# Kernel tuning notes

Hardware: AMD Instinct MI355X
Metric: run time of the kernel (lower is better)

## Reference

```python
import jax, jax.numpy as jnp
import numpy as np

N = 50000      # nodes
E = 800000     # edges (avg degree 16)
IN = 128       # in_channels
HID = 32       # hidden_channels per head
HEADS = 4
OUT = 64       # out_channels (last layer, heads=1, concat=False)
ED = 32        # edge_dim
NEG_SLOPE = 0.2


def _gatv2_layer(x, src, dst, ea, Wl, bl, Wr, br, We, att, bias, concat):
    """PyG GATv2Conv: lin_l -> source (x_j), lin_r -> target (x_i),
    score = att . leaky_relu(x_i + x_j + lin_edge(edge_attr)), segment-softmax over dst,
    out = scatter_add(alpha * x_j) per head, then concat or mean heads, plus bias."""
    n = x.shape[0]
    H, C = att.shape
    xl = (x @ Wl + bl).reshape(-1, H, C)   # [N,H,C] source transform
    xr = (x @ Wr + br).reshape(-1, H, C)   # [N,H,C] target transform
    ee = (ea @ We).reshape(-1, H, C)       # [E,H,C] edge transform
    m = jax.nn.leaky_relu(xl[src] + xr[dst] + ee, NEG_SLOPE)  # [E,H,C]
    a = jnp.einsum('ehc,hc->eh', m, att)   # [E,H] attention logits
    amax = jax.ops.segment_max(a, dst, num_segments=n)        # [N,H]
    ex = jnp.exp(a - amax[dst])
    den = jax.ops.segment_sum(ex, dst, num_segments=n)        # [N,H]
    alpha = ex / (den[dst] + 1e-16)        # [E,H] segment softmax
    out = jax.ops.segment_sum(xl[src] * alpha[..., None], dst, num_segments=n)  # [N,H,C]
    out = out.reshape(n, H * C) if concat else out.mean(axis=1)
    return out + bias


def setup_inputs() -> dict:
    key = jax.random.key(0)
    ks = jax.random.split(key, 20)
    s = 0.05
    HC = HEADS * HID
    inp = {
        'x': jax.random.normal(ks[0], (N, IN), jnp.float32),
        'edge_index': jax.random.randint(ks[1], (2, E), 0, N, jnp.int32),
        'edge_attr': jax.random.normal(ks[2], (E, ED), jnp.float32),
        # layer 1: GATv2Conv(IN -> HID, heads=HEADS, concat=True, edge_dim=ED)
        'Wl1': jax.random.normal(ks[3], (IN, HC), jnp.float32) * s,
        'bl1': jnp.zeros((HC,), jnp.float32),
        'Wr1': jax.random.normal(ks[4], (IN, HC), jnp.float32) * s,
        'br1': jnp.zeros((HC,), jnp.float32),
        'We1': jax.random.normal(ks[5], (ED, HC), jnp.float32) * s,
        'att1': jax.random.normal(ks[6], (HEADS, HID), jnp.float32) * s,
        'bias1': jnp.zeros((HC,), jnp.float32),
        # layer 2: GATv2Conv(HC -> OUT, heads=1, concat=False, edge_dim=ED)
        'Wl2': jax.random.normal(ks[7], (HC, OUT), jnp.float32) * s,
        'bl2': jnp.zeros((OUT,), jnp.float32),
        'Wr2': jax.random.normal(ks[8], (HC, OUT), jnp.float32) * s,
        'br2': jnp.zeros((OUT,), jnp.float32),
        'We2': jax.random.normal(ks[9], (ED, OUT), jnp.float32) * s,
        'att2': jax.random.normal(ks[10], (1, OUT), jnp.float32) * s,
        'bias2': jnp.zeros((OUT,), jnp.float32),
    }
    return inp


def reference(x, edge_index, edge_attr, Wl1, bl1, Wr1, br1, We1, att1, bias1,
              Wl2, bl2, Wr2, br2, We2, att2, bias2):
    src, dst = edge_index[0], edge_index[1]
    h = _gatv2_layer(x, src, dst, edge_attr, Wl1, bl1, Wr1, br1, We1, att1, bias1, concat=True)
    h = jax.nn.elu(h)
    out = _gatv2_layer(h, src, dst, edge_attr, Wl2, bl2, Wr2, br2, We2, att2, bias2, concat=False)
    return out
```

## Files before the change

### kernel.cpp

```cpp
#include <hip/hip_runtime.h>
#include <stdint.h>

#define N_NODES 50000
#define N_EDGES 800000

struct Ptrs { const void* p[16]; int n[16]; };

typedef __attribute__((ext_vector_type(8))) short bf16x8;
typedef __attribute__((ext_vector_type(4))) float f32x4;

__device__ __forceinline__ float bf2f(unsigned short u){
  union { unsigned int i; float f; } v; v.i = ((unsigned int)u) << 16; return v.f;
}
__device__ __forceinline__ float lo16(unsigned int u){ union { unsigned int i; float f; } v; v.i = u << 16; return v.f; }
__device__ __forceinline__ float hi16(unsigned int u){ union { unsigned int i; float f; } v; v.i = u & 0xffff0000u; return v.f; }
__device__ __forceinline__ unsigned short f2bf(float f){
  if (!(f == f)) return 0;
  unsigned int x = __float_as_uint(f);
  unsigned int r = (x + 0x7fffu + ((x >> 16) & 1u)) >> 16;
  return (unsigned short)r;
}
__device__ __forceinline__ float fin(float v){
  if (!(v == v)) return 0.f;
  return fminf(fmaxf(v, -1e30f), 1e30f);
}
__device__ __forceinline__ float loadF(const void* p, int f32, size_t idx){
  return f32 ? ((const float*)p)[idx] : bf2f(((const unsigned short*)p)[idx]);
}

__global__ __launch_bounds__(256) void k_detect(Ptrs tl, int* __restrict__ flags,
                                                int* __restrict__ counts, int* __restrict__ pad16)
{
  if (blockIdx.x >= 16) {
    int i = (blockIdx.x - 16) * 256 + threadIdx.x;
    if (i < N_NODES) counts[i] = 0;
    if (blockIdx.x == 16 && threadIdx.x < 16) pad16[threadIdx.x] = 0;
    return;
  }
  __shared__ int red[256];
  int b = blockIdx.x, t = threadIdx.x;
  const unsigned short* p = (const unsigned short*)tl.p[b];
  int n = tl.n[b]; if (n > 16384) n = 16384;
  int crazy = 0;
  for (int i = t; i < n; i += 256) {
    unsigned short u = p[i];
    if (u) {
      int ex = (u >> 7) & 0xFF;
      if (ex == 0xFF || ex < 0x60) crazy++;
    }
  }
  red[t] = crazy; __syncthreads();
  for (int off = 128; off; off >>= 1) { if (t < off) red[t] += red[t + off]; __syncthreads(); }
  if (t == 0) flags[b] = (red[0] * 10 > n) ? 1 : 0;
}

__global__ __launch_bounds__(256) void k_gemm1(
    const void* __restrict__ x,
    const void* __restrict__ Wl, const void* __restrict__ bl,
    const void* __restrict__ Wr, const void* __restrict__ br,
    const int* __restrict__ flags,
    unsigned int* __restrict__ xlp, unsigned int* __restrict__ xrp)
{
  __shared__ __align__(16) char smem[17408];
  unsigned short* xh  = (unsigned short*)smem;
  unsigned short* xlo = (unsigned short*)(smem + 8704);
  float* outb = (float*)smem;
  const void* W  = blockIdx.y ? Wr : Wl;
  const void* bb = blockIdx.y ? br : bl;
  int fW = blockIdx.y ? flags[4] : flags[2];
  int fB = blockIdx.y ? flags[5] : flags[3];
  int fX = flags[0];
  unsigned int* outp = blockIdx.y ? xrp : xlp;
  int tid = threadIdx.x;
  int row0 = blockIdx.x * 32;
  for (int i = tid * 4; i < 32 * 128; i += 1024) {
    int r = i >> 7, k = i & 127;
    int row = row0 + r;
    float4 v = make_float4(0.f, 0.f, 0.f, 0.f);
    if (row < N_NODES) {
      if (fX) v = *(const float4*)((const float*)x + (size_t)row * 128 + k);
      else {
        uint2 u = *(const uint2*)((const unsigned short*)x + (size_t)row * 128 + k);
        v.x = lo16(u.x); v.y = hi16(u.x); v.z = lo16(u.y); v.w = hi16(u.y);
      }
    }
    unsigned short h0 = f2bf(v.x), h1 = f2bf(v.y), h2 = f2bf(v.z), h3 = f2bf(v.w);
    *(ushort4*)(xh + r * 136 + k) = make_ushort4(h0, h1, h2, h3);
    ushort4 lv;
    lv.x = f2bf(v.x - bf2f(h0)); lv.y = f2bf(v.y - bf2f(h1));
    lv.z = f2bf(v.z - bf2f(h2)); lv.w = f2bf(v.w - bf2f(h3));
    *(ushort4*)(xlo + r * 136 + k) = lv;
  }
  int lane = tid & 63, wv = tid >> 6;
  int idx16 = lane & 15, quad = lane >> 4;
  bf16x8 bfr[2][4];
#pragma unroll
  for (int ct = 0; ct < 2; ct++) {
#pragma unroll
    for (int kc = 0; kc < 4; kc++) {
      int col = wv * 32 + ct * 16 + idx16;
      unsigned short tmp[8];
#pragma unroll
      for (int j = 0; j < 8; j++) {
        int kk = kc * 32 + quad * 8 + j;
        tmp[j] = fW ? f2bf(((const float*)W)[(size_t)kk * 128 + col])
                    : ((const unsigned short*)W)[(size_t)kk * 128 + col];
      }
      bfr[ct][kc] = *(const bf16x8*)tmp;
    }
  }
  __syncthreads();
  f32x4 acc[2][2];
#pragma unroll
  for (int rt = 0; rt < 2; rt++)
#pragma unroll
    for (int ct = 0; ct < 2; ct++)
      acc[rt][ct] = (f32x4){0.f, 0.f, 0.f, 0.f};
#pragma unroll
  for (int kc = 0; kc < 4; kc++) {
#pragma unroll
    for (int rt = 0; rt < 2; rt++) {
      bf16x8 ah = *(const bf16x8*)(xh  + (rt * 16 + idx16) * 136 + kc * 32 + quad * 8);
      bf16x8 al = *(const bf16x8*)(xlo + (rt * 16 + idx16) * 136 + kc * 32 + quad * 8);
#pragma unroll
      for (int ct = 0; ct < 2; ct++) {
        acc[rt][ct] = __builtin_amdgcn_mfma_f32_16x16x32_bf16(ah, bfr[ct][kc], acc[rt][ct], 0, 0, 0);
        acc[rt][ct] = __builtin_amdgcn_mfma_f32_16x16x32_bf16(al, bfr[ct][kc], acc[rt][ct], 0, 0, 0);
      }
    }
  }
  __syncthreads();
#pragma unroll
  for (int rt = 0; rt < 2; rt++)
#pragma unroll
    for (int ct = 0; ct < 2; ct++)
#pragma unroll
      for (int r = 0; r < 4; r++)
        outb[(rt * 16 + quad * 4 + r) * 132 + wv * 32 + ct * 16 + idx16] = acc[rt][ct][r];
  __syncthreads();
  int r = tid >> 3, cg = tid & 7;
  float a2[16];
#pragma unroll
  for (int j = 0; j < 8; j++) {
    a2[j]     = outb[r * 132 + cg * 8 + j];
    a2[8 + j] = outb[r * 132 + 64 + cg * 8 + j];
  }
  int row = row0 + r;
  if (row < N_NODES) {
    unsigned int* op = outp + (size_t)row * 64;
    int tt = cg >> 1, qb = (cg & 1) * 2;
    unsigned int ou[4];
#pragma unroll
    for (int t = 0; t < 4; t++) {
      float f0 = fin(a2[2 * t]     + loadF(bb, fB, cg * 8 + 2 * t));
      float f1 = fin(a2[2 * t + 1] + loadF(bb, fB, cg * 8 + 2 * t + 1));
      ou[t] = (unsigned)f2bf(f0) | ((unsigned)f2bf(f1) << 16);
    }
    *(uint2*)(op + qb * 16 + tt * 2)       = make_uint2(ou[0], ou[1]);
    *(uint2*)(op + (qb + 1) * 16 + tt * 2) = make_uint2(ou[2], ou[3]);
#pragma unroll
    for (int t = 0; t < 4; t++) {
      float f0 = fin(a2[8 + 2 * t]     + loadF(bb, fB, 64 + cg * 8 + 2 * t));
      float f1 = fin(a2[8 + 2 * t + 1] + loadF(bb, fB, 64 + cg * 8 + 2 * t + 1));
      ou[t] = (unsigned)f2bf(f0) | ((unsigned)f2bf(f1) << 16);
    }
    *(uint2*)(op + qb * 16 + 8 + tt * 2)       = make_uint2(ou[0], ou[1]);
    *(uint2*)(op + (qb + 1) * 16 + 8 + tt * 2) = make_uint2(ou[2], ou[3]);
  }
}

__global__ __launch_bounds__(256) void k_gemm2(
    const float* __restrict__ h,
    const void* __restrict__ Wl, const void* __restrict__ bl,
    const void* __restrict__ Wr, const void* __restrict__ br,
    const int* __restrict__ flags,
    unsigned int* __restrict__ xlp, unsigned int* __restrict__ xrp)
{
  __shared__ __align__(16) char smem[17408];
  unsigned short* hh  = (unsigned short*)smem;
  unsigned short* hlo = (unsigned short*)(smem + 8704);
  float* outb = (float*)smem;
  const void* W  = blockIdx.y ? Wr : Wl;
  const void* bb = blockIdx.y ? br : bl;
  int fW = blockIdx.y ? flags[11] : flags[9];
  int fB = blockIdx.y ? flags[12] : flags[10];
  unsigned int* outp = blockIdx.y ? xrp : xlp;
  int tid = threadIdx.x;
  int row0 = blockIdx.x * 32;
  for (int i = tid * 4; i < 32 * 128; i += 1024) {
    int r = i >> 7, k = i & 127;
    int row = row0 + r;
    float4 v = make_float4(0.f, 0.f, 0.f, 0.f);
    if (row < N_NODES) v = *(const float4*)(h + (size_t)row * 128 + k);
    unsigned short h0 = f2bf(v.x), h1 = f2bf(v.y), h2 = f2bf(v.z), h3 = f2bf(v.w);
    *(ushort4*)(hh + r * 136 + k) = make_ushort4(h0, h1, h2, h3);
    ushort4 lv;
    lv.x = f2bf(v.x - bf2f(h0)); lv.y = f2bf(v.y - bf2f(h1));
    lv.z = f2bf(v.z - bf2f(h2)); lv.w = f2bf(v.w - bf2f(h3));
    *(ushort4*)(hlo + r * 136 + k) = lv;
  }
  int lane = tid & 63, wv = tid >> 6;
  int idx16 = lane & 15, quad = lane >> 4;
  bf16x8 bfr[4];
#pragma unroll
  for (int kc = 0; kc < 4; kc++) {
    int col = wv * 16 + idx16;
    unsigned short tmp[8];
#pragma unroll
    for (int j = 0; j < 8; j++) {
      int kk = kc * 32 + quad * 8 + j;
      tmp[j] = fW ? f2bf(((const float*)W)[(size_t)kk * 64 + col])
                  : ((const unsigned short*)W)[(size_t)kk * 64 + col];
    }
    bfr[kc] = *(const bf16x8*)tmp;
  }
  __syncthreads();
  f32x4 acc[2];
  acc[0] = (f32x4){0.f, 0.f, 0.f, 0.f};
  acc[1] = (f32x4){0.f, 0.f, 0.f, 0.f};
#pragma unroll
  for (int kc = 0; kc < 4; kc++) {
#pragma unroll
    for (int rt = 0; rt < 2; rt++) {
      bf16x8 ah = *(const bf16x8*)(hh  + (rt * 16 + idx16) * 136 + kc * 32 + quad * 8);
      bf16x8 al = *(const bf16x8*)(hlo + (rt * 16 + idx16) * 136 + kc * 32 + quad * 8);
      acc[rt] = __builtin_amdgcn_mfma_f32_16x16x32_bf16(ah, bfr[kc], acc[rt], 0, 0, 0);
      acc[rt] = __builtin_amdgcn_mfma_f32_16x16x32_bf16(al, bfr[kc], acc[rt], 0, 0, 0);
    }
  }
  __syncthreads();
#pragma unroll
  for (int rt = 0; rt < 2; rt++)
#pragma unroll
    for (int r = 0; r < 4; r++)
      outb[(rt * 16 + quad * 4 + r) * 68 + wv * 16 + idx16] = acc[rt][r];
  __syncthreads();
  int r = tid >> 3, cg = tid & 7;
  float a2[8];
#pragma unroll
  for (int j = 0; j < 8; j++) a2[j] = outb[r * 68 + cg * 8 + j];
  int row = row0 + r;
  if (row < N_NODES) {
    unsigned int* op = outp + (size_t)row * 32;
    int tt = cg >> 1, qb = (cg & 1) * 2;
    unsigned int ou[4];
#pragma unroll
    for (int t = 0; t < 4; t++) {
      float f0 = fin(a2[2 * t]     + loadF(bb, fB, cg * 8 + 2 * t));
      float f1 = fin(a2[2 * t + 1] + loadF(bb, fB, cg * 8 + 2 * t + 1));
      ou[t] = (unsigned)f2bf(f0) | ((unsigned)f2bf(f1) << 16);
    }
    *(uint2*)(op + qb * 8 + tt * 2)       = make_uint2(ou[0], ou[1]);
    *(uint2*)(op + (qb + 1) * 8 + tt * 2) = make_uint2(ou[2], ou[3]);
  }
}

__global__ __launch_bounds__(256) void k_hist(const int* __restrict__ ei, int* __restrict__ counts)
{
  int e = blockIdx.x * 256 + threadIdx.x;
  if (e < N_EDGES) {
    int d = ei[N_EDGES + e]; if ((unsigned)d >= N_NODES) d = 0;
    atomicAdd(&counts[d], 1);
  }
}

__global__ __launch_bounds__(256) void k_scan1(const int* __restrict__ counts,
                                               int* __restrict__ row_ptr, int* __restrict__ bsum)
{
  __shared__ int lds[256];
  int t = threadIdx.x;
  int base = blockIdx.x * 1024 + t * 4;
  int c0 = (base + 0) < N_NODES ? counts[base + 0] : 0;
  int c1 = (base + 1) < N_NODES ? counts[base + 1] : 0;
  int c2 = (base + 2) < N_NODES ? counts[base + 2] : 0;
  int c3 = (base + 3) < N_NODES ? counts[base + 3] : 0;
  int s = c0 + c1 + c2 + c3;
  lds[t] = s; __syncthreads();
  for (int off = 1; off < 256; off <<= 1) {
    int v = (t >= off) ? lds[t - off] : 0;
    __syncthreads();
    lds[t] += v;
    __syncthreads();
  }
  int incl = lds[t];
  int excl = incl - s;
  if (base + 0 < N_NODES) row_ptr[base + 0] = excl;
  if (base + 1 < N_NODES) row_ptr[base + 1] = excl + c0;
  if (base + 2 < N_NODES) row_ptr[base + 2] = excl + c0 + c1;
  if (base + 3 < N_NODES) row_ptr[base + 3] = excl + c0 + c1 + c2;
  if (t == 255) bsum[blockIdx.x] = incl;
}

__global__ __launch_bounds__(64) void k_scan2(int* __restrict__ bsum, int nb)
{
  __shared__ int l[64];
  int t = threadIdx.x;
  if (t < nb) l[t] = bsum[t];
  __syncthreads();
  if (t == 0) { int run = 0; for (int i = 0; i < nb; i++) { int v = l[i]; l[i] = run; run += v; } }
  __syncthreads();
  if (t < nb) bsum[t] = l[t];
}

__global__ __launch_bounds__(256) void k_scan3(int* __restrict__ row_ptr, int* __restrict__ cursor,
                                               const int* __restrict__ bsum)
{
  int t = threadIdx.x;
  int base = blockIdx.x * 1024 + t * 4;
  int add = bsum[blockIdx.x];
#pragma unroll
  for (int j = 0; j < 4; j++) {
    int i = base + j;
    if (i < N_NODES) { int v = row_ptr[i] + add; row_ptr[i] = v; cursor[i] = v; }
  }
  if (blockIdx.x == 0 && t == 0) row_ptr[N_NODES] = N_EDGES;
}

__global__ __launch_bounds__(256) void k_scatter(const int* __restrict__ ei,
                                                 int* __restrict__ cursor,
                                                 int* __restrict__ srcs,
                                                 const void* __restrict__ ea,
                                                 const int* __restrict__ flags,
                                                 unsigned short* __restrict__ eap)
{
  int e = blockIdx.x * 256 + threadIdx.x;
  if (e >= N_EDGES) return;
  int d = ei[N_EDGES + e]; if ((unsigned)d >= N_NODES) d = 0;
  int s = ei[e];           if ((unsigned)s >= N_NODES) s = 0;
  int p = atomicAdd(&cursor[d], 1);
  if ((unsigned)p >= N_EDGES) return;
  srcs[p] = s;
  unsigned short* op = eap + (size_t)p * 32;
  if (flags[1]) {
    const float* ip = (const float*)ea + (size_t)e * 32;
#pragma unroll
    for (int q = 0; q < 2; q++) {
      float4 a = *(const float4*)(ip + q * 16);
      float4 b = *(const float4*)(ip + q * 16 + 4);
      float4 c = *(const float4*)(ip + q * 16 + 8);
      float4 dd = *(const float4*)(ip + q * 16 + 12);
      uint4 u0, u1;
      u0.x = (unsigned)f2bf(a.x) | ((unsigned)f2bf(a.y) << 16);
      u0.y = (unsigned)f2bf(a.z) | ((unsigned)f2bf(a.w) << 16);
      u0.z = (unsigned)f2bf(b.x) | ((unsigned)f2bf(b.y) << 16);
      u0.w = (unsigned)f2bf(b.z) | ((unsigned)f2bf(b.w) << 16);
      u1.x = (unsigned)f2bf(c.x) | ((unsigned)f2bf(c.y) << 16);
      u1.y = (unsigned)f2bf(c.z) | ((unsigned)f2bf(c.w) << 16);
      u1.z = (unsigned)f2bf(dd.x) | ((unsigned)f2bf(dd.y) << 16);
      u1.w = (unsigned)f2bf(dd.z) | ((unsigned)f2bf(dd.w) << 16);
      *(uint4*)(op + q * 16) = u0;
      *(uint4*)(op + q * 16 + 8) = u1;
    }
  } else {
    const uint4* ip = (const uint4*)((const unsigned short*)ea + (size_t)e * 32);
#pragma unroll
    for (int q = 0; q < 4; q++) *(uint4*)(op + q * 8) = ip[q];
  }
}

__global__ __launch_bounds__(256) void k_fuse1(
    const unsigned short* __restrict__ eap, const int* __restrict__ srcs,
    const int* __restrict__ row_ptr,
    const unsigned int* __restrict__ xlp, const unsigned int* __restrict__ xrp,
    const void* __restrict__ We, const void* __restrict__ att,
    const void* __restrict__ bias, const int* __restrict__ flags,
    float* __restrict__ hout)
{
  __shared__ unsigned short wt[128 * 34];
  __shared__ float at[128];
  int tid = threadIdx.x;
  {
    int f = flags[6];
    for (int i2 = tid; i2 < 4096; i2 += 256) {
      int k = i2 >> 7, c = i2 & 127;
      wt[c * 34 + k] = f ? f2bf(((const float*)We)[i2]) : ((const unsigned short*)We)[i2];
    }
  }
  if (tid < 128) at[tid] = loadF(att, flags[7], tid);
  __syncthreads();
  int lane = tid & 63;
  int idx16 = lane & 15, quad = lane >> 4;
  int t_s = (lane & 15) >> 1, b_s = lane & 1;
  int un = t_s * 8 + quad * 2 + b_s;
  int hd = un >> 4;
  bf16x8 af[8];
#pragma unroll
  for (int t = 0; t < 8; t++)
    af[t] = *(const bf16x8*)(wt + (t * 16 + idx16) * 34 + quad * 8);
  int wv = tid >> 6;
#pragma unroll 1
  for (int rep = 0; rep < 2; rep++) {
    int i = blockIdx.x * 8 + rep * 4 + wv;
    int p0 = row_ptr[i], p1 = row_ptr[i + 1];
    uint2 rv[8];
#pragma unroll
    for (int t4 = 0; t4 < 4; t4++) {
      uint4 u = *(const uint4*)(xrp + (size_t)i * 64 + quad * 16 + t4 * 4);
      rv[2 * t4]     = make_uint2(u.x, u.y);
      rv[2 * t4 + 1] = make_uint2(u.z, u.w);
    }
    float acc0 = 0.f, acc1 = 0.f, den = 0.f;
    for (int jb = p0; jb < p1; jb += 16) {
      int j = jb + idx16;
      int act = j < p1;
      int jc = act ? j : p0;
      int s = srcs[jc];
      bf16x8 bfrag = *(const bf16x8*)(eap + (size_t)jc * 32 + quad * 8);
      uint2 xv[8];
#pragma unroll
      for (int t4 = 0; t4 < 4; t4++) {
        uint4 u = *(const uint4*)(xlp + (size_t)s * 64 + quad * 16 + t4 * 4);
        xv[2 * t4]     = make_uint2(u.x, u.y);
        xv[2 * t4 + 1] = make_uint2(u.z, u.w);
      }
      float ph0 = 0.f, ph1 = 0.f, ph2 = 0.f, ph3 = 0.f;
#pragma unroll
      for (int t = 0; t < 8; t++) {
        float4 av = *(const float4*)(at + t * 16 + quad * 4);
        uint2 r = rv[t];
        f32x4 c = {0.f, 0.f, 0.f, 0.f};
        c = __builtin_amdgcn_mfma_f32_16x16x32_bf16(af[t], bfrag, c, 0, 0, 0);
        float z0 = c[0] + lo16(xv[t].x) + lo16(r.x);
        float z1 = c[1] + hi16(xv[t].x) + hi16(r.x);
        float z2 = c[2] + lo16(xv[t].y) + lo16(r.y);
        float z3 = c[3] + hi16(xv[t].y) + hi16(r.y);
        z0 = z0 > 0.f ? z0 : 0.2f * z0;
        z1 = z1 > 0.f ? z1 : 0.2f * z1;
        z2 = z2 > 0.f ? z2 : 0.2f * z2;
        z3 = z3 > 0.f ? z3 : 0.2f * z3;
        float pp = fmaf(av.x, z0, fmaf(av.y, z1, fmaf(av.z, z2, av.w * z3)));
        if (t < 2)      ph0 += pp;
        else if (t < 4) ph1 += pp;
        else if (t < 6) ph2 += pp;
        else            ph3 += pp;
      }
      ph0 += __shfl_xor(ph0, 16, 64); ph0 += __shfl_xor(ph0, 32, 64);
      ph1 += __shfl_xor(ph1, 16, 64); ph1 += __shfl_xor(ph1, 32, 64);
      ph2 += __shfl_xor(ph2, 16, 64); ph2 += __shfl_xor(ph2, 32, 64);
      ph3 += __shfl_xor(ph3, 16, 64); ph3 += __shfl_xor(ph3, 32, 64);
      float w0 = act ? __expf(fminf(fin(ph0), 25.f)) : 0.f;
      float w1 = act ? __expf(fminf(fin(ph1), 25.f)) : 0.f;
      float w2 = act ? __expf(fminf(fin(ph2), 25.f)) : 0.f;
      float w3 = act ? __expf(fminf(fin(ph3), 25.f)) : 0.f;
      float wsel = quad == 0 ? w0 : quad == 1 ? w1 : quad == 2 ? w2 : w3;
      int sjl[16];
      float wjv[16];
#pragma unroll
      for (int q = 0; q < 16; q++) sjl[q] = __shfl(s, q, 64);
#pragma unroll
      for (int q = 0; q < 16; q++) wjv[q] = __shfl(wsel, hd * 16 + q, 64);
#pragma unroll
      for (int q = 0; q < 16; q++) {
        unsigned int v = xlp[(size_t)sjl[q] * 64 + lane];
        acc0 = fmaf(wjv[q], lo16(v), acc0);
        acc1 = fmaf(wjv[q], hi16(v), acc1);
        den += wjv[q];
      }
    }
    float inv = 1.f / (den + 1e-16f);
    int fB = flags[8];
    int ch = un * 2;
    float o0 = fin(fmaf(acc0, inv, loadF(bias, fB, ch)));
    float o1 = fin(fmaf(acc1, inv, loadF(bias, fB, ch + 1)));
    o0 = o0 > 0.f ? o0 : __expf(o0) - 1.f;
    o1 = o1 > 0.f ? o1 : __expf(o1) - 1.f;
    *(float2*)(hout + (size_t)i * 128 + ch) = make_float2(o0, o1);
  }
}

__global__ __launch_bounds__(256) void k_fuse2(
    const unsigned short* __restrict__ eap, const int* __restrict__ srcs,
    const int* __restrict__ row_ptr,
    const unsigned int* __restrict__ xlp, const unsigned int* __restrict__ xrp,
    const void* __restrict__ We, const void* __restrict__ att,
    const void* __restrict__ bias, const int* __restrict__ flags,
    void* __restrict__ out)
{
  __shared__ unsigned short wt[64 * 34];
  __shared__ float at[64];
  int tid = threadIdx.x;
  {
    int f = flags[13];
    for (int i2 = tid; i2 < 2048; i2 += 256) {
      int k = i2 >> 6, c = i2 & 63;
      wt[c * 34 + k] = f ? f2bf(((const float*)We)[i2]) : ((const unsigned short*)We)[i2];
    }
  }
  if (tid < 64) at[tid] = loadF(att, flags[14], tid);
  __syncthreads();
  int lane = tid & 63;
  int idx16 = lane & 15, quad = lane >> 4;
  int l5 = lane & 31;
  int q_s = l5 >> 3, t2 = (l5 & 7) >> 1, b2 = l5 & 1;
  int un = t2 * 8 + q_s * 2 + b2;
  int halfe = lane >> 5;
  bf16x8 af[4];
#pragma unroll
  for (int t = 0; t < 4; t++)
    af[t] = *(const bf16x8*)(wt + (t * 16 + idx16) * 34 + quad * 8);
  int wv = tid >> 6;
#pragma unroll 1
  for (int rep = 0; rep < 2; rep++) {
    int i = blockIdx.x * 8 + rep * 4 + wv;
    int p0 = row_ptr[i], p1 = row_ptr[i + 1];
    uint2 rv[4];
#pragma unroll
    for (int k = 0; k < 2; k++) {
      uint4 u = *(const uint4*)(xrp + (size_t)i * 32 + quad * 8 + k * 4);
      rv[2 * k]     = make_uint2(u.x, u.y);
      rv[2 * k + 1] = make_uint2(u.z, u.w);
    }
    float acc0 = 0.f, acc1 = 0.f, den = 0.f;
    for (int jb = p0; jb < p1; jb += 16) {
      int j = jb + idx16;
      int act = j < p1;
      int jc = act ? j : p0;
      int s = srcs[jc];
      bf16x8 bfrag = *(const bf16x8*)(eap + (size_t)jc * 32 + quad * 8);
      uint2 xv[4];
#pragma unroll
      for (int k = 0; k < 2; k++) {
        uint4 u = *(const uint4*)(xlp + (size_t)s * 32 + quad * 8 + k * 4);
        xv[2 * k]     = make_uint2(u.x, u.y);
        xv[2 * k + 1] = make_uint2(u.z, u.w);
      }
      float ph = 0.f;
#pragma unroll
      for (int t = 0; t < 4; t++) {
        float4 av = *(const float4*)(at + t * 16 + quad * 4);
        uint2 r = rv[t];
        f32x4 c = {0.f, 0.f, 0.f, 0.f};
        c = __builtin_amdgcn_mfma_f32_16x16x32_bf16(af[t], bfrag, c, 0, 0, 0);
        float z0 = c[0] + lo16(xv[t].x) + lo16(r.x);
        float z1 = c[1] + hi16(xv[t].x) + hi16(r.x);
        float z2 = c[2] + lo16(xv[t].y) + lo16(r.y);
        float z3 = c[3] + hi16(xv[t].y) + hi16(r.y);
        z0 = z0 > 0.f ? z0 : 0.2f * z0;
        z1 = z1 > 0.f ? z1 : 0.2f * z1;
        z2 = z2 > 0.f ? z2 : 0.2f * z2;
        z3 = z3 > 0.f ? z3 : 0.2f * z3;
        ph += fmaf(av.x, z0, fmaf(av.y, z1, fmaf(av.z, z2, av.w * z3)));
      }
      ph += __shfl_xor(ph, 16, 64);
      ph += __shfl_xor(ph, 32, 64);
      float wsel = act ? __expf(fminf(fin(ph), 25.f)) : 0.f;
      int sjl[8];
      float wjv[8];
#pragma unroll
      for (int q = 0; q < 8; q++) {
        int qq = 2 * q + halfe;
        sjl[q] = __shfl(s, qq, 64);
        wjv[q] = __shfl(wsel, qq, 64);
      }
#pragma unroll
      for (int q = 0; q < 8; q++) {
        unsigned int v = xlp[(size_t)sjl[q] * 32 + l5];
        acc0 = fmaf(wjv[q], lo16(v), acc0);
        acc1 = fmaf(wjv[q], hi16(v), acc1);
        den += wjv[q];
      }
    }
    acc0 += __shfl_xor(acc0, 32, 64);
    acc1 += __shfl_xor(acc1, 32, 64);
    den  += __shfl_xor(den, 32, 64);
    if (lane < 32) {
      float inv = 1.f / (den + 1e-16f);
      int fB = flags[15];
      int ch = un * 2;
      float o0 = fin(fmaf(acc0, inv, loadF(bias, fB, ch)));
      float o1 = fin(fmaf(acc1, inv, loadF(bias, fB, ch + 1)));
      if (flags[0]) {
        *(float2*)((float*)out + (size_t)i * 64 + ch) = make_float2(o0, o1);
      } else {
        unsigned int u = (unsigned)f2bf(o0) | ((unsigned)f2bf(o1) << 16);
        *(unsigned int*)((unsigned short*)out + (size_t)i * 64 + ch) = u;
      }
    }
  }
}

extern "C" void kernel_launch(void* const* d_in, const int* in_sizes, int n_in,
                              void* d_out, int out_size, void* d_ws, size_t ws_size,
                              hipStream_t stream)
{
  (void)n_in; (void)out_size; (void)ws_size;
  const void* x    = d_in[0];
  const int*  ei   = (const int*)d_in[1];
  const void* ea   = d_in[2];
  const void* Wl1  = d_in[3];
  const void* bl1  = d_in[4];
  const void* Wr1  = d_in[5];
  const void* br1  = d_in[6];
  const void* We1  = d_in[7];
  const void* att1 = d_in[8];
  const void* bias1= d_in[9];
  const void* Wl2  = d_in[10];
  const void* bl2  = d_in[11];
  const void* Wr2  = d_in[12];
  const void* br2  = d_in[13];
  const void* We2  = d_in[14];
  const void* att2 = d_in[15];
  const void* bias2= d_in[16];

  char* ws = (char*)d_ws;
  size_t off = 0;
  auto take = [&](size_t bytes) -> char* {
    char* p = ws + off;
    off += (bytes + 255) & ~(size_t)255;
    return p;
  };
  unsigned int* xl1p = (unsigned int*)take((size_t)N_NODES * 64 * 4);
  unsigned int* xr1p = (unsigned int*)take((size_t)N_NODES * 64 * 4);
  float* hbuf   = (float*)take((size_t)N_NODES * 128 * 4);
  unsigned short* eap = (unsigned short*)take((size_t)(N_EDGES + 16) * 32 * 2);
  int*   counts = (int*)  take((size_t)N_NODES * 4);
  int*   row_ptr= (int*)  take((size_t)(N_NODES + 1) * 4);
  int*   cursor = (int*)  take((size_t)N_NODES * 4);
  int*   srcs   = (int*)  take((size_t)(N_EDGES + 16) * 4);
  int*   bsum   = (int*)  take(64 * 4);
  int*   flags  = (int*)  take(64 * 4);
  unsigned int* xl2p = xl1p;
  unsigned int* xr2p = xr1p;

  Ptrs tl;
  const int map[16] = {0, 2, 3, 4, 5, 6, 7, 8, 9, 10, 11, 12, 13, 14, 15, 16};
  for (int j = 0; j < 16; j++) { tl.p[j] = d_in[map[j]]; tl.n[j] = in_sizes[map[j]]; }

  int nb = (N_NODES + 1023) / 1024;
  int zblocks = (N_NODES + 255) / 256;
  k_detect<<<16 + zblocks, 256, 0, stream>>>(tl, flags, counts, srcs + N_EDGES);
  k_gemm1<<<dim3((N_NODES + 31) / 32, 2), 256, 0, stream>>>(x, Wl1, bl1, Wr1, br1, flags, xl1p, xr1p);
  k_hist<<<(N_EDGES + 255) / 256, 256, 0, stream>>>(ei, counts);
  k_scan1<<<nb, 256, 0, stream>>>(counts, row_ptr, bsum);
  k_scan2<<<1, 64, 0, stream>>>(bsum, nb);
  k_scan3<<<nb, 256, 0, stream>>>(row_ptr, cursor, bsum);
  k_scatter<<<(N_EDGES + 255) / 256, 256, 0, stream>>>(ei, cursor, srcs, ea, flags, eap);
  k_fuse1<<<N_NODES / 8, 256, 0, stream>>>(eap, srcs, row_ptr, xl1p, xr1p, We1, att1, bias1, flags, hbuf);
  k_gemm2<<<dim3((N_NODES + 31) / 32, 2), 256, 0, stream>>>(hbuf, Wl2, bl2, Wr2, br2, flags, xl2p, xr2p);
  k_fuse2<<<N_NODES / 8, 256, 0, stream>>>(eap, srcs, row_ptr, xl2p, xr2p, We2, att2, bias2, flags, d_out);
}
```

Before: 657.7 us.

## Merge scan kernels, stage target rows in LDS, prefetch neighbor rows early

Fuses the single-block bsum scan into the offset-add kernel: each block reduces the preceding block sums with wave shuffles, which removes one launch. In both aggregation kernels the target-node xr rows are staged in shared memory instead of registers. The gathered source-row loads for the weighted sum are now issued before the MFMA and attention computation, so their latency overlaps that math. The cost is higher register pressure from the 16 prefetched values, plus extra LDS reads inside the inner loop.

```diff
diff --git a/kernel.cpp b/kernel.cpp
--- a/kernel.cpp
+++ b/kernel.cpp
@@ -291,23 +291,21 @@
   if (t == 255) bsum[blockIdx.x] = incl;
 }
 
-__global__ __launch_bounds__(64) void k_scan2(int* __restrict__ bsum, int nb)
-{
-  __shared__ int l[64];
+__global__ __launch_bounds__(256) void k_scan23(int* __restrict__ row_ptr, int* __restrict__ cursor,
+                                                const int* __restrict__ bsum, int nb)
+{
+  __shared__ int sadd;
   int t = threadIdx.x;
-  if (t < nb) l[t] = bsum[t];
-  __syncthreads();
-  if (t == 0) { int run = 0; for (int i = 0; i < nb; i++) { int v = l[i]; l[i] = run; run += v; } }
-  __syncthreads();
-  if (t < nb) bsum[t] = l[t];
-}
-
-__global__ __launch_bounds__(256) void k_scan3(int* __restrict__ row_ptr, int* __restrict__ cursor,
-                                               const int* __restrict__ bsum)
-{
-  int t = threadIdx.x;
+  if (t < 64) {
+    int v = (t < nb && t < (int)blockIdx.x) ? bsum[t] : 0;
+    v += __shfl_xor(v, 1, 64);  v += __shfl_xor(v, 2, 64);
+    v += __shfl_xor(v, 4, 64);  v += __shfl_xor(v, 8, 64);
+    v += __shfl_xor(v, 16, 64); v += __shfl_xor(v, 32, 64);
+    if (t == 0) sadd = v;
+  }
+  __syncthreads();
+  int add = sadd;
   int base = blockIdx.x * 1024 + t * 4;
-  int add = bsum[blockIdx.x];
 #pragma unroll
   for (int j = 0; j < 4; j++) {
     int i = base + j;
@@ -368,6 +366,7 @@
 {
   __shared__ unsigned short wt[128 * 34];
   __shared__ float at[128];
+  __shared__ __align__(16) unsigned int xr_s[8 * 64];
   int tid = threadIdx.x;
   {
     int f = flags[6];
@@ -377,6 +376,8 @@
     }
   }
   if (tid < 128) at[tid] = loadF(att, flags[7], tid);
+  for (int i2 = tid; i2 < 512; i2 += 256)
+    xr_s[i2] = xrp[(size_t)(blockIdx.x * 8 + (i2 >> 6)) * 64 + (i2 & 63)];
   __syncthreads();
   int lane = tid & 63;
   int idx16 = lane & 15, quad = lane >> 4;
@@ -390,15 +391,10 @@
   int wv = tid >> 6;
 #pragma unroll 1
   for (int rep = 0; rep < 2; rep++) {
-    int i = blockIdx.x * 8 + rep * 4 + wv;
+    int loc = rep * 4 + wv;
+    int i = blockIdx.x * 8 + loc;
     int p0 = row_ptr[i], p1 = row_ptr[i + 1];
-    uint2 rv[8];
-#pragma unroll
-    for (int t4 = 0; t4 < 4; t4++) {
-      uint4 u = *(const uint4*)(xrp + (size_t)i * 64 + quad * 16 + t4 * 4);
-      rv[2 * t4]     = make_uint2(u.x, u.y);
-      rv[2 * t4 + 1] = make_uint2(u.z, u.w);
-    }
+    const unsigned int* xr_row = xr_s + loc * 64;
     float acc0 = 0.f, acc1 = 0.f, den = 0.f;
     for (int jb = p0; jb < p1; jb += 16) {
       int j = jb + idx16;
@@ -413,11 +409,17 @@
         xv[2 * t4]     = make_uint2(u.x, u.y);
         xv[2 * t4 + 1] = make_uint2(u.z, u.w);
       }
+      int sjl[16];
+#pragma unroll
+      for (int q = 0; q < 16; q++) sjl[q] = __shfl(s, q, 64);
+      unsigned int vq[16];
+#pragma unroll
+      for (int q = 0; q < 16; q++) vq[q] = xlp[(size_t)sjl[q] * 64 + lane];
       float ph0 = 0.f, ph1 = 0.f, ph2 = 0.f, ph3 = 0.f;
 #pragma unroll
       for (int t = 0; t < 8; t++) {
         float4 av = *(const float4*)(at + t * 16 + quad * 4);
-        uint2 r = rv[t];
+        uint2 r = *(const uint2*)(xr_row + quad * 16 + t * 2);
         f32x4 c = {0.f, 0.f, 0.f, 0.f};
         c = __builtin_amdgcn_mfma_f32_16x16x32_bf16(af[t], bfrag, c, 0, 0, 0);
         float z0 = c[0] + lo16(xv[t].x) + lo16(r.x);
@@ -443,18 +445,12 @@
       float w2 = act ? __expf(fminf(fin(ph2), 25.f)) : 0.f;
       float w3 = act ? __expf(fminf(fin(ph3), 25.f)) : 0.f;
       float wsel = quad == 0 ? w0 : quad == 1 ? w1 : quad == 2 ? w2 : w3;
-      int sjl[16];
-      float wjv[16];
-#pragma unroll
-      for (int q = 0; q < 16; q++) sjl[q] = __shfl(s, q, 64);
-#pragma unroll
-      for (int q = 0; q < 16; q++) wjv[q] = __shfl(wsel, hd * 16 + q, 64);
 #pragma unroll
       for (int q = 0; q < 16; q++) {
-        unsigned int v = xlp[(size_t)sjl[q] * 64 + lane];
-        acc0 = fmaf(wjv[q], lo16(v), acc0);
-        acc1 = fmaf(wjv[q], hi16(v), acc1);
-        den += wjv[q];
+        float wq = __shfl(wsel, hd * 16 + q, 64);
+        acc0 = fmaf(wq, lo16(vq[q]), acc0);
+        acc1 = fmaf(wq, hi16(vq[q]), acc1);
+        den += wq;
       }
     }
     float inv = 1.f / (den + 1e-16f);
@@ -478,6 +474,7 @@
 {
   __shared__ unsigned short wt[64 * 34];
   __shared__ float at[64];
+  __shared__ __align__(16) unsigned int xr_s[8 * 32];
   int tid = threadIdx.x;
   {
     int f = flags[13];
@@ -487,6 +484,10 @@
     }
   }
   if (tid < 64) at[tid] = loadF(att, flags[14], tid);
+  if (tid < 256) {
+    int i2 = tid;
+    if (i2 < 256) xr_s[i2] = xrp[(size_t)(blockIdx.x * 8 + (i2 >> 5)) * 32 + (i2 & 31)];
+  }
   __syncthreads();
   int lane = tid & 63;
   int idx16 = lane & 15, quad = lane >> 4;
@@ -501,15 +502,10 @@
   int wv = tid >> 6;
 #pragma unroll 1
   for (int rep = 0; rep < 2; rep++) {
-    int i = blockIdx.x * 8 + rep * 4 + wv;
+    int loc = rep * 4 + wv;
+    int i = blockIdx.x * 8 + loc;
     int p0 = row_ptr[i], p1 = row_ptr[i + 1];
-    uint2 rv[4];
-#pragma unroll
-    for (int k = 0; k < 2; k++) {
-      uint4 u = *(const uint4*)(xrp + (size_t)i * 32 + quad * 8 + k * 4);
-      rv[2 * k]     = make_uint2(u.x, u.y);
-      rv[2 * k + 1] = make_uint2(u.z, u.w);
-    }
+    const unsigned int* xr_row = xr_s + loc * 32;
     float acc0 = 0.f, acc1 = 0.f, den = 0.f;
     for (int jb = p0; jb < p1; jb += 16) {
       int j = jb + idx16;
@@ -524,11 +520,17 @@
         xv[2 * k]     = make_uint2(u.x, u.y);
         xv[2 * k + 1] = make_uint2(u.z, u.w);
       }
+      int sjl[8];
+#pragma unroll
+      for (int q = 0; q < 8; q++) sjl[q] = __shfl(s, 2 * q + halfe, 64);
+      unsigned int vq[8];
+#pragma unroll
+      for (int q = 0; q < 8; q++) vq[q] = xlp[(size_t)sjl[q] * 32 + l5];
       float ph = 0.f;
 #pragma unroll
       for (int t = 0; t < 4; t++) {
         float4 av = *(const float4*)(at + t * 16 + quad * 4);
-        uint2 r = rv[t];
+        uint2 r = *(const uint2*)(xr_row + quad * 8 + t * 2);
         f32x4 c = {0.f, 0.f, 0.f, 0.f};
         c = __builtin_amdgcn_mfma_f32_16x16x32_bf16(af[t], bfrag, c, 0, 0, 0);
         float z0 = c[0] + lo16(xv[t].x) + lo16(r.x);
@@ -544,20 +546,12 @@
       ph += __shfl_xor(ph, 16, 64);
       ph += __shfl_xor(ph, 32, 64);
       float wsel = act ? __expf(fminf(fin(ph), 25.f)) : 0.f;
-      int sjl[8];
-      float wjv[8];
 #pragma unroll
       for (int q = 0; q < 8; q++) {
-        int qq = 2 * q + halfe;
-        sjl[q] = __shfl(s, qq, 64);
-        wjv[q] = __shfl(wsel, qq, 64);
-      }
-#pragma unroll
-      for (int q = 0; q < 8; q++) {
-        unsigned int v = xlp[(size_t)sjl[q] * 32 + l5];
-        acc0 = fmaf(wjv[q], lo16(v), acc0);
-        acc1 = fmaf(wjv[q], hi16(v), acc1);
-        den += wjv[q];
+        float wq = __shfl(wsel, 2 * q + halfe, 64);
+        acc0 = fmaf(wq, lo16(vq[q]), acc0);
+        acc1 = fmaf(wq, hi16(vq[q]), acc1);
+        den += wq;
       }
     }
     acc0 += __shfl_xor(acc0, 32, 64);
@@ -632,8 +626,7 @@
   k_gemm1<<<dim3((N_NODES + 31) / 32, 2), 256, 0, stream>>>(x, Wl1, bl1, Wr1, br1, flags, xl1p, xr1p);
   k_hist<<<(N_EDGES + 255) / 256, 256, 0, stream>>>(ei, counts);
   k_scan1<<<nb, 256, 0, stream>>>(counts, row_ptr, bsum);
-  k_scan2<<<1, 64, 0, stream>>>(bsum, nb);
-  k_scan3<<<nb, 256, 0, stream>>>(row_ptr, cursor, bsum);
+  k_scan23<<<nb, 256, 0, stream>>>(row_ptr, cursor, bsum, nb);
   k_scatter<<<(N_EDGES + 255) / 256, 256, 0, stream>>>(ei, cursor, srcs, ea, flags, eap);
   k_fuse1<<<N_NODES / 8, 256, 0, stream>>>(eap, srcs, row_ptr, xl1p, xr1p, We1, att1, bias1, flags, hbuf);
   k_gemm2<<<dim3((N_NODES + 31) / 32, 2), 256, 0, stream>>>(hbuf, Wl2, bl2, Wr2, br2, flags, xl2p, xr2p);
```

Measured after the change: 640.7 us. 2.6% less time.
